# Kernel optimization log

Hardware: AMD Instinct MI355X
Metric: run time of the kernel (lower is better)

## Reference

```python
import jax, jax.numpy as jnp
import numpy as np

N_ANGLES = 180
N_DETECTORS = 256


def _bilinear_sample(img, x, y):
    """Bilinear sample img[y, x]; zero outside. img: [H, W]; x, y: any shape."""
    H, W = img.shape
    x0 = jnp.floor(x)
    y0 = jnp.floor(y)
    xi = x0.astype(jnp.int32)
    yi = y0.astype(jnp.int32)
    wx = x - x0
    wy = y - y0

    def get(ix, iy):
        valid = (ix >= 0) & (ix < W) & (iy >= 0) & (iy < H)
        ixc = jnp.clip(ix, 0, W - 1)
        iyc = jnp.clip(iy, 0, H - 1)
        return jnp.where(valid, img[iyc, ixc], jnp.zeros((), img.dtype))

    v00 = get(xi, yi)
    v01 = get(xi + 1, yi)
    v10 = get(xi, yi + 1)
    v11 = get(xi + 1, yi + 1)
    return (v00 * (1.0 - wx) + v01 * wx) * (1.0 - wy) + (v10 * (1.0 - wx) + v11 * wx) * wy


def setup_inputs() -> dict:
    key = jax.random.key(0)
    inputs = jax.random.uniform(key, (8, 256, 256, 1), dtype=jnp.float32)
    return {"inputs": inputs}


def reference(inputs):
    # Parallel-beam forward Radon transform (forwardproject).
    # inputs: [B, H, W, 1] image batch -> sinogram [B, n_angles, n_detectors, 1]
    B, H, W, _ = inputs.shape
    A, D = N_ANGLES, N_DETECTORS
    T = H  # integration samples along each ray

    theta = jnp.linspace(0.0, jnp.pi, A, endpoint=False, dtype=inputs.dtype)
    cos_t = jnp.cos(theta)[:, None, None]  # [A,1,1]
    sin_t = jnp.sin(theta)[:, None, None]

    s = (jnp.arange(D, dtype=inputs.dtype) - (D - 1) / 2.0)[None, :, None]  # detector offsets
    t = (jnp.arange(T, dtype=inputs.dtype) - (T - 1) / 2.0)[None, None, :]  # along-ray offsets

    cx = (W - 1) / 2.0
    cy = (H - 1) / 2.0
    # sample coords for every (angle, detector, ray-step): [A, D, T]
    x = cx + s * cos_t - t * sin_t
    y = cy + s * sin_t + t * cos_t

    imgs = inputs[..., 0]  # [B, H, W]
    vals = jax.vmap(lambda im: _bilinear_sample(im, x, y))(imgs)  # [B, A, D, T]
    sino = vals.sum(axis=-1)  # ray integral (unit step length)
    return sino[..., None]  # [B, A, D, 1]
```

## Files before the change

kernel.cpp:

```cpp
#include <hip/hip_runtime.h>
#include <math.h>

#define NA    180
#define HB    9
#define KB    29
#define P0C   261
#define P0R   273
#define P1R   261
#define P1C   261
#define TR    12
#define TSZ   (261 * TR)
#define OUTN  (8 * NA * 256)

typedef _Float16 h2  __attribute__((ext_vector_type(2)));
typedef _Float16 h8  __attribute__((ext_vector_type(8)));
typedef __fp16   hf2 __attribute__((ext_vector_type(2)));

__device__ __forceinline__ h2 pkrtz(float a, float b) {
    hf2 t = __builtin_amdgcn_cvt_pkrtz(a, b);
    return __builtin_bit_cast(h2, t);
}
__device__ __forceinline__ float fdot2f(h2 a, h2 b, float c) {
#if __has_builtin(__builtin_amdgcn_fdot2)
    return __builtin_amdgcn_fdot2(__builtin_bit_cast(hf2, a),
                                  __builtin_bit_cast(hf2, b), c, false);
#else
    return c + (float)a.x * (float)b.x + (float)a.y * (float)b.y;
#endif
}
__device__ __forceinline__ float imc(const float* im, int y, int x) {
    return ((unsigned)y < 256u && (unsigned)x < 256u) ? im[(y << 8) + x] : 0.0f;
}

__global__ __launch_bounds__(256) void prep_kernel(
    const float* __restrict__ img, uint4* __restrict__ P0,
    uint4* __restrict__ P1, float* __restrict__ out, float* __restrict__ tab)
{
    const int tid = threadIdx.x;
    const int row = blockIdx.x;
    const int mb  = blockIdx.y;

    if (mb == 0) {
        for (int i = row * 256 + tid; i < OUTN; i += P0R * 256) out[i] = 0.0f;
    }
    if (mb == 1 && row == 0 && tid < NA) {
        const float theta = (float)tid * ((float)M_PI / (float)NA);
        tab[tid]      = cosf(theta);
        tab[tid + NA] = sinf(theta);
    }

    const int bg = mb & 1;
    const float* im0 = img + ((size_t)(bg * 4) << 16);

    if (mb < 2) {
        const int v = row - 4;
        uint4* dst = P0 + (size_t)(bg * P0R + row) * P0C;
        for (int j = tid; j < P0C; j += 256) {
            const int u = j - 2;
            h8 t;
            t[0] = (_Float16)imc(im0,             v, u); t[1] = (_Float16)imc(im0,             v + 1, u);
            t[2] = (_Float16)imc(im0 + (1 << 16), v, u); t[3] = (_Float16)imc(im0 + (1 << 16), v + 1, u);
            t[4] = (_Float16)imc(im0 + (2 << 16), v, u); t[5] = (_Float16)imc(im0 + (2 << 16), v + 1, u);
            t[6] = (_Float16)imc(im0 + (3 << 16), v, u); t[7] = (_Float16)imc(im0 + (3 << 16), v + 1, u);
            dst[j] = __builtin_bit_cast(uint4, t);
        }
    } else {
        if (row >= P1R) return;
        const int u = row - 2;
        uint4* dst = P1 + (size_t)(bg * P1R + row) * P1C;
        for (int j = tid; j < P1C; j += 256) {
            const int v = j - 2;
            h8 t;
            t[0] = (_Float16)imc(im0,             u, v); t[1] = (_Float16)imc(im0,             u, v + 1);
            t[2] = (_Float16)imc(im0 + (1 << 16), u, v); t[3] = (_Float16)imc(im0 + (1 << 16), u, v + 1);
            t[4] = (_Float16)imc(im0 + (2 << 16), u, v); t[5] = (_Float16)imc(im0 + (2 << 16), u, v + 1);
            t[6] = (_Float16)imc(im0 + (3 << 16), u, v); t[7] = (_Float16)imc(im0 + (3 << 16), u, v + 1);
            dst[j] = __builtin_bit_cast(uint4, t);
        }
    }
}

#define SAMPLE(JV, UV, VPV, A0, A1, A2, A3)                                   \
    {                                                                         \
        const float ucl = fminf(fmaxf((UV), -1.5f), 257.5f);                  \
        const float uf = floorf(ucl);                                         \
        const float wu = ucl - uf;                                            \
        const float vf = floorf(VPV);                                         \
        const float wv = (VPV) - vf;                                          \
        const float vfc = fminf(fmaxf(vf, -2.0f), 9.0f);                      \
        int idx;                                                              \
        if (MODEX) idx = (int)fmaf(uf, 12.0f, vfc) + 26;                      \
        else       idx = (int)fmaf(vfc, 261.0f, uf) + 524;                    \
        const h8 A8 = __builtin_bit_cast(h8, s_tile[idx]);                    \
        const h8 B8 = __builtin_bit_cast(h8, s_tile[idx + (MODEX ? TR : 1)]); \
        const h2 wu2 = pkrtz(wu, wu);                                         \
        const h8 wu8 = __builtin_shufflevector(wu2, wu2, 0,1,0,1,0,1,0,1);    \
        const h8 tb8 = (B8 - A8) * wu8 + A8;                                  \
        h2 wv2 = pkrtz(1.0f - wv, wv);                                        \
        wv2 = ((unsigned)(JV) < span) ? wv2 : hz;                             \
        A0 = fdot2f(__builtin_shufflevector(tb8, tb8, 0, 1), wv2, A0);        \
        A1 = fdot2f(__builtin_shufflevector(tb8, tb8, 2, 3), wv2, A1);        \
        A2 = fdot2f(__builtin_shufflevector(tb8, tb8, 4, 5), wv2, A2);        \
        A3 = fdot2f(__builtin_shufflevector(tb8, tb8, 6, 7), wv2, A3);        \
    }

template<bool MODEX>
__device__ __forceinline__ void radon_body(
    const uint4* __restrict__ Pbase,
    float* __restrict__ out, const float* __restrict__ tab,
    uint4* s_tile, int tid, int b0, int p, int gi)
{
    const int lo = -2 + p * HB;

    if (!MODEX) {
        const uint4* src = Pbase + (size_t)(lo + 2) * P0C;
        for (int i = tid; i < TSZ; i += 256) s_tile[i] = src[i];
    } else {
        for (int i = tid; i < TSZ; i += 256) {
            const int r = i / TR;
            const int c = i - r * TR;
            const int pj = lo + c;
            uint4 val = make_uint4(0u, 0u, 0u, 0u);
            if ((unsigned)pj < (unsigned)P1C)
                val = Pbase[(size_t)r * P1C + pj];
            s_tile[i] = val;
        }
    }
    __syncthreads();

    const float detf = (float)tid - 127.5f;
    const float lof = (float)lo;
    const h2 hz = {};

    for (int g = 0; g < 7; ++g) {
        const int ai = gi * 7 + g;
        int a;
        if (MODEX) { if (ai >= 89) break; a = 46 + ai; }
        else       { a = (ai <= 45) ? ai : 89 + ai; }

        const float c = tab[a];
        const float s = tab[a + NA];

        const float xc = 127.5f + detf * c + 127.5f * s;
        const float yc = 127.5f + detf * s - 127.5f * c;

        const float ucst = MODEX ? yc : xc;
        const float vcst = MODEX ? xc : yc;
        const float du   = MODEX ? c  : -s;
        const float dv   = MODEX ? -s : c;

        const float inv = 1.0f / dv;
        const float f1 = (lof - vcst) * inv;
        const float f2 = (lof + (float)HB - vcst) * inv;
        const float fmn = fminf(f1, f2);
        const float fmx = fmaxf(f1, f2);
        int kmin, kend;
        if (dv > 0.0f) { kmin = (int)ceilf(fmn);      kend = (int)ceilf(fmx); }
        else           { kmin = (int)floorf(fmn) + 1; kend = (int)floorf(fmx) + 1; }

        const int len = kend - kmin;
        const int jlo = max(0, -kmin);
        const int jhi = min(len, 256 - kmin);
        const int spani = max(0, jhi - jlo);
        if (!__any(spani > 0)) continue;
        const unsigned span = (unsigned)spani;

        const int kstart = kmin + jlo;
        const int Lmax = (int)((float)HB * fabsf(inv)) + 2;

        float u  = fmaf((float)kstart, du, ucst);
        float vp = fmaf((float)kstart, dv, vcst - lof);
        const float du2 = du + du, dv2 = dv + dv;

        float a0 = 0.f, a1 = 0.f, a2 = 0.f, a3 = 0.f;
        float b0a = 0.f, b1a = 0.f, b2a = 0.f, b3a = 0.f;

        int j = 0;
        for (; j + 1 < Lmax; j += 2) {
            SAMPLE(j,     u,      vp,      a0, a1, a2, a3);
            SAMPLE(j + 1, u + du, vp + dv, b0a, b1a, b2a, b3a);
            u += du2; vp += dv2;
        }
        if (j < Lmax) SAMPLE(j, u, vp, a0, a1, a2, a3);

        if (spani > 0) {
            float* o = &out[((b0 * NA + a) << 8) + tid];
            atomicAdd(o,                 a0 + b0a);
            atomicAdd(o + (NA << 8),     a1 + b1a);
            atomicAdd(o + 2 * (NA << 8), a2 + b2a);
            atomicAdd(o + 3 * (NA << 8), a3 + b3a);
        }
    }
}

__global__ __launch_bounds__(256, 3) void radon_kernel(
    const uint4* __restrict__ P0, const uint4* __restrict__ P1,
    float* __restrict__ out, const float* __restrict__ tab)
{
    __shared__ uint4 s_tile[TSZ];
    const int tid = threadIdx.x;
    const int bg  = blockIdx.x;
    const int p   = blockIdx.y;
    const int gid = blockIdx.z;
    const int b0  = bg * 4;
    if (gid < 13)
        radon_body<false>(P0 + (size_t)bg * P0R * P0C, out, tab, s_tile, tid, b0, p, gid);
    else
        radon_body<true>(P1 + (size_t)bg * P1R * P1C, out, tab, s_tile, tid, b0, p, gid - 13);
}

extern "C" void kernel_launch(void* const* d_in, const int* in_sizes, int n_in,
                              void* d_out, int out_size, void* d_ws, size_t ws_size,
                              hipStream_t stream) {
    const float* img = (const float*)d_in[0];
    float* out = (float*)d_out;

    uint4* P0 = (uint4*)d_ws;
    uint4* P1 = P0 + (size_t)2 * P0R * P0C;
    float* tab = (float*)(P1 + (size_t)2 * P1R * P1C);

    prep_kernel<<<dim3(P0R, 4), 256, 0, stream>>>(img, P0, P1, out, tab);
    radon_kernel<<<dim3(2, KB, 26), 256, 0, stream>>>(P0, P1, out, tab);
}
```

Measured before the change: 108.9 us.

## Store transposed image pack row-major so both ray families share tile loads

The P1 packed buffer, used for near-vertical angles, is now laid out with the same row-major shape as P0 (273 rows by 261 columns of transposed pixels). The MODEX path can then load its shared tile as a contiguous copy, with no per-element division and bounds check, and can index the tile the same way as the other path. This removes strided, gathered global loads and extra index arithmetic in the tile fill. It relies on the transposed buffer and the MODEX coordinate meaning matching exactly; if the two do not agree, results will be wrong.

```diff
diff --git a/kernel.cpp b/kernel.cpp
--- a/kernel.cpp
+++ b/kernel.cpp
@@ -6,10 +6,8 @@
 #define KB    29
 #define P0C   261
 #define P0R   273
-#define P1R   261
-#define P1C   261
-#define TR    12
-#define TSZ   (261 * TR)
+#define TROWS 12
+#define TSZ   (P0C * TROWS)
 #define OUTN  (8 * NA * 256)
 
 typedef _Float16 h2  __attribute__((ext_vector_type(2)));
@@ -51,9 +49,9 @@
 
     const int bg = mb & 1;
     const float* im0 = img + ((size_t)(bg * 4) << 16);
+    const int v = row - 4;
 
     if (mb < 2) {
-        const int v = row - 4;
         uint4* dst = P0 + (size_t)(bg * P0R + row) * P0C;
         for (int j = tid; j < P0C; j += 256) {
             const int u = j - 2;
@@ -65,11 +63,9 @@
             dst[j] = __builtin_bit_cast(uint4, t);
         }
     } else {
-        if (row >= P1R) return;
-        const int u = row - 2;
-        uint4* dst = P1 + (size_t)(bg * P1R + row) * P1C;
-        for (int j = tid; j < P1C; j += 256) {
-            const int v = j - 2;
+        uint4* dst = P1 + (size_t)(bg * P0R + row) * P0C;
+        for (int j = tid; j < P0C; j += 256) {
+            const int u = j - 2;
             h8 t;
             t[0] = (_Float16)imc(im0,             u, v); t[1] = (_Float16)imc(im0,             u, v + 1);
             t[2] = (_Float16)imc(im0 + (1 << 16), u, v); t[3] = (_Float16)imc(im0 + (1 << 16), u, v + 1);
@@ -88,11 +84,9 @@
         const float vf = floorf(VPV);                                         \
         const float wv = (VPV) - vf;                                          \
         const float vfc = fminf(fmaxf(vf, -2.0f), 9.0f);                      \
-        int idx;                                                              \
-        if (MODEX) idx = (int)fmaf(uf, 12.0f, vfc) + 26;                      \
-        else       idx = (int)fmaf(vfc, 261.0f, uf) + 524;                    \
+        const int idx = (int)fmaf(vfc, 261.0f, uf) + 524;                     \
         const h8 A8 = __builtin_bit_cast(h8, s_tile[idx]);                    \
-        const h8 B8 = __builtin_bit_cast(h8, s_tile[idx + (MODEX ? TR : 1)]); \
+        const h8 B8 = __builtin_bit_cast(h8, s_tile[idx + 1]);                \
         const h2 wu2 = pkrtz(wu, wu);                                         \
         const h8 wu8 = __builtin_shufflevector(wu2, wu2, 0,1,0,1,0,1,0,1);    \
         const h8 tb8 = (B8 - A8) * wu8 + A8;                                  \
@@ -112,19 +106,9 @@
 {
     const int lo = -2 + p * HB;
 
-    if (!MODEX) {
+    {
         const uint4* src = Pbase + (size_t)(lo + 2) * P0C;
         for (int i = tid; i < TSZ; i += 256) s_tile[i] = src[i];
-    } else {
-        for (int i = tid; i < TSZ; i += 256) {
-            const int r = i / TR;
-            const int c = i - r * TR;
-            const int pj = lo + c;
-            uint4 val = make_uint4(0u, 0u, 0u, 0u);
-            if ((unsigned)pj < (unsigned)P1C)
-                val = Pbase[(size_t)r * P1C + pj];
-            s_tile[i] = val;
-        }
     }
     __syncthreads();
 
@@ -206,7 +190,7 @@
     if (gid < 13)
         radon_body<false>(P0 + (size_t)bg * P0R * P0C, out, tab, s_tile, tid, b0, p, gid);
     else
-        radon_body<true>(P1 + (size_t)bg * P1R * P1C, out, tab, s_tile, tid, b0, p, gid - 13);
+        radon_body<true>(P1 + (size_t)bg * P0R * P0C, out, tab, s_tile, tid, b0, p, gid - 13);
 }
 
 extern "C" void kernel_launch(void* const* d_in, const int* in_sizes, int n_in,
@@ -217,7 +201,7 @@
 
     uint4* P0 = (uint4*)d_ws;
     uint4* P1 = P0 + (size_t)2 * P0R * P0C;
-    float* tab = (float*)(P1 + (size_t)2 * P1R * P1C);
+    float* tab = (float*)(P1 + (size_t)2 * P0R * P0C);
 
     prep_kernel<<<dim3(P0R, 4), 256, 0, stream>>>(img, P0, P1, out, tab);
     radon_kernel<<<dim3(2, KB, 26), 256, 0, stream>>>(P0, P1, out, tab);
```

Result: slower. 111.6 us (+2.4%).
